# Optimization experiments

Hardware: AMD Instinct MI355X
Metric: run time of the kernel (lower is better)

## Reference

```python
import jax, jax.numpy as jnp
import numpy as np

N = 1500                 # number of proposals
NUM_CLASSES = 81         # COCO: background + 80
NMS_THRESH = 0.5
SCORE_THRESH = 0.05
MAX_DET = 100            # config.test.max_det
BBOX_REG_WEIGHTS = jnp.array([10.0, 10.0, 5.0, 5.0], dtype=jnp.float32)


def setup_inputs() -> dict:
    key = jax.random.key(0)
    k1, k2, k3 = jax.random.split(key, 3)
    H, W = 800.0, 1333.0
    # realistic proposals: random centers / sizes inside the image
    cx = jax.random.uniform(jax.random.fold_in(k1, 0), (N,)) * W
    cy = jax.random.uniform(jax.random.fold_in(k1, 1), (N,)) * H
    bw = jax.random.uniform(jax.random.fold_in(k1, 2), (N,)) * 200.0 + 16.0
    bh = jax.random.uniform(jax.random.fold_in(k1, 3), (N,)) * 200.0 + 16.0
    bottom_rois = jnp.stack(
        [jnp.zeros((N,)), cx - 0.5 * bw, cy - 0.5 * bh, cx + 0.5 * bw, cy + 0.5 * bh],
        axis=1).astype(jnp.float32)
    bbox_delta = (jax.random.normal(k2, (N, 4 * NUM_CLASSES)) * 0.5).astype(jnp.float32)
    cls_prob = jax.nn.softmax(jax.random.normal(k3, (N, NUM_CLASSES)) * 2.0, axis=-1).astype(jnp.float32)
    im_info = jnp.array([[H, W, 1.0]], dtype=jnp.float32)
    return {"bottom_rois": bottom_rois, "bbox_delta": bbox_delta,
            "cls_prob": cls_prob, "im_info": im_info}


def _decode_boxes(rois, deltas, im_info):
    # rois [N,4], deltas [N,4C] -> clipped boxes [N,C,4] (legacy +1 convention)
    x1, y1, x2, y2 = rois[:, 0], rois[:, 1], rois[:, 2], rois[:, 3]
    w = x2 - x1 + 1.0
    h = y2 - y1 + 1.0
    cx = x1 + 0.5 * w
    cy = y1 + 0.5 * h
    d = deltas.reshape(deltas.shape[0], -1, 4) / BBOX_REG_WEIGHTS  # [N,C,4]
    pcx = cx[:, None] + w[:, None] * d[..., 0]
    pcy = cy[:, None] + h[:, None] * d[..., 1]
    pw = w[:, None] * jnp.exp(d[..., 2])
    ph = h[:, None] * jnp.exp(d[..., 3])
    boxes = jnp.stack([pcx - 0.5 * pw, pcy - 0.5 * ph,
                       pcx + 0.5 * pw - 1.0, pcy + 0.5 * ph - 1.0], axis=-1)
    hw = im_info[0, :2]  # [height, width]
    lim = jnp.stack([hw[1] - 1.0, hw[0] - 1.0, hw[1] - 1.0, hw[0] - 1.0])
    return jnp.clip(boxes, 0.0, lim)


def _pairwise_iou(b):
    # b [N,4], legacy +1 areas (matches gpu_nms)
    x1, y1, x2, y2 = b[:, 0], b[:, 1], b[:, 2], b[:, 3]
    area = (x2 - x1 + 1.0) * (y2 - y1 + 1.0)
    iw = jnp.maximum(jnp.minimum(x2[:, None], x2[None, :]) - jnp.maximum(x1[:, None], x1[None, :]) + 1.0, 0.0)
    ih = jnp.maximum(jnp.minimum(y2[:, None], y2[None, :]) - jnp.maximum(y1[:, None], y1[None, :]) + 1.0, 0.0)
    inter = iw * ih
    return inter / (area[:, None] + area[None, :] - inter)


def _nms_one_class(boxes, scores):
    # boxes [N,4], scores [N] -> score-sorted boxes/scores + keep mask
    valid = scores > SCORE_THRESH
    order = jnp.argsort(-scores)
    b = boxes[order]
    s = scores[order]
    v = valid[order]
    iou = jax.lax.stop_gradient(_pairwise_iou(b))  # used only in comparisons

    def body(suppressed, i):
        keep_i = v[i] & ~suppressed[i]
        suppressed = suppressed | (keep_i & (iou[i] > NMS_THRESH))
        return suppressed, keep_i

    _, keep = jax.lax.scan(body, jnp.zeros((b.shape[0],), bool), jnp.arange(b.shape[0]))
    return b, s, keep


def reference(bottom_rois, bbox_delta, cls_prob, im_info):
    boxes = _decode_boxes(bottom_rois[:, 1:], bbox_delta, im_info)  # [N,C,4]
    C = cls_prob.shape[1]
    boxes_fg = jnp.swapaxes(boxes, 0, 1)[1:]   # [C-1,N,4]
    scores_fg = cls_prob.T[1:]                 # [C-1,N]
    b, s, keep = jax.vmap(_nms_one_class)(boxes_fg, scores_fg)
    # image-level max_det cap (>= kth score, as in source)
    flat = jnp.where(keep, s, -jnp.inf).reshape(-1)
    n_keep = keep.sum()
    kth = jax.lax.top_k(flat, MAX_DET)[0][-1]
    keep = keep & jnp.where(n_keep > MAX_DET, s >= kth, True)
    cls_idx = jnp.broadcast_to(jnp.arange(1, C)[:, None], s.shape)
    zeros = jnp.zeros_like(s[..., None])
    dets = jnp.concatenate([zeros, b, s[..., None]], axis=-1)  # [C-1,N,6]
    dets = jnp.where(keep[..., None], dets, 0.0).reshape(-1, 6)
    return dets, cls_idx.reshape(-1), keep.reshape(-1)
```

## Files before the change

kernel.cpp:

```cpp
#include <hip/hip_runtime.h>
#include <math.h>

#pragma clang fp contract(off)

#define N_ROIS     1500
#define NUM_CLS    81
#define FG         80
#define MAXC       1536
#define NMS_T      0.5f
#define SCORE_T    0.05f
#define MAX_DET    100
#define TOTAL      (FG * N_ROIS)
#define TPB        256
#define K1_BLOCKS  256
#define K2_TPB     1024
#define NCHUNK     ((N_ROIS + TPB - 1) / TPB)
#define SUBCAP     8192

__device__ __forceinline__ unsigned f2s(float f) {
    unsigned u = __float_as_uint(f);
    return (u & 0x80000000u) ? ~u : (u | 0x80000000u);
}
__device__ __forceinline__ float s2f(unsigned u) {
    return __uint_as_float((u & 0x80000000u) ? (u & 0x7FFFFFFFu) : ~u);
}

__global__ __launch_bounds__(TPB) void nms_k1(
    const float* __restrict__ rois,
    const float* __restrict__ deltas,
    const float* __restrict__ prob,
    const float* __restrict__ iminfo,
    float4* __restrict__ keptBox,
    int*    __restrict__ keptRow,
    float*  __restrict__ keptScore,
    int*    __restrict__ ctrs,
    float*  __restrict__ out)
{
    const int tid  = threadIdx.x;
    const int lane = tid & 63;
    const int wv   = tid >> 6;
    const int b    = blockIdx.x;

    if (b >= FG) {
        const float4 z4 = make_float4(0.f, 0.f, 0.f, 0.f);
        const int stride = (K1_BLOCKS - FG) * TPB;
        int g = (b - FG) * TPB + tid;

        float4* dets4 = (float4*)out;
        for (int i = g; i < TOTAL * 6 / 4; i += stride) dets4[i] = z4;

        float4* cls4  = (float4*)(out + (size_t)TOTAL * 6);
        float4* keep4 = (float4*)(out + (size_t)TOTAL * 7);
        for (int i = g; i < TOTAL / 4; i += stride) {
            float fc = (float)((i * 4) / N_ROIS + 1);
            cls4[i]  = make_float4(fc, fc, fc, fc);
            keep4[i] = z4;
        }
        return;
    }

    __shared__ unsigned long long key[MAXC];
    __shared__ unsigned long long skey[MAXC];
    __shared__ float4 box4[MAXC];
    __shared__ float  areaA[MAXC];
    __shared__ unsigned char keepf[MAXC], supp[MAXC];
    __shared__ int mcnt;

    const int c = b + 1;
    const int cbase = b * N_ROIS;

    if (tid == 0) mcnt = 0;
    __syncthreads();

    float sv[NCHUNK];
    #pragma unroll
    for (int t = 0; t < NCHUNK; ++t) {
        int i = t * TPB + tid;
        sv[t] = (i < N_ROIS) ? prob[i * NUM_CLS + c] : 0.0f;
    }
    #pragma unroll
    for (int t = 0; t < NCHUNK; ++t) {
        int i = t * TPB + tid;
        bool val = (i < N_ROIS) && (sv[t] > SCORE_T);
        unsigned long long m = __ballot(val);
        int base = 0;
        if (lane == 0 && m) base = atomicAdd(&mcnt, __popcll(m));
        base = __shfl(base, 0, 64);
        if (val) {
            int pos = base + __popcll(m & ((1ull << lane) - 1ull));
            key[pos] = ((unsigned long long)(~f2s(sv[t])) << 32) | (unsigned)i;
        }
    }
    __syncthreads();
    const int M = mcnt;
    if (M == 0) return;

    for (int i = tid; i < M; i += TPB) {
        unsigned long long kk = key[i];
        int cnt = 0;
        #pragma unroll 4
        for (int j = 0; j < M; ++j) cnt += (int)(key[j] < kk);
        skey[cnt] = kk;
    }
    __syncthreads();

    const float Hm1 = iminfo[0] - 1.0f;
    const float Wm1 = iminfo[1] - 1.0f;
    for (int k = tid; k < M; k += TPB) {
        unsigned long long kk = skey[k];
        int i = (int)(kk & 0xFFFFFFFFu);
        const float* rp = rois + i * 5;
        float x1 = rp[1], y1 = rp[2], x2 = rp[3], y2 = rp[4];
        float w  = x2 - x1 + 1.0f;
        float h  = y2 - y1 + 1.0f;
        float cx = x1 + 0.5f * w;
        float cy = y1 + 0.5f * h;
        const float* dp = deltas + i * (4 * NUM_CLS) + c * 4;
        float dx = dp[0] / 10.0f, dy = dp[1] / 10.0f;
        float dw = dp[2] / 5.0f,  dh = dp[3] / 5.0f;
        float pcx = cx + w * dx;
        float pcy = cy + h * dy;
        float pw  = w * expf(dw);
        float ph  = h * expf(dh);
        float a1 = pcx - 0.5f * pw;
        float a2 = pcy - 0.5f * ph;
        float a3 = pcx + 0.5f * pw - 1.0f;
        float a4 = pcy + 0.5f * ph - 1.0f;
        a1 = fminf(fmaxf(a1, 0.0f), Wm1);
        a2 = fminf(fmaxf(a2, 0.0f), Hm1);
        a3 = fminf(fmaxf(a3, 0.0f), Wm1);
        a4 = fminf(fmaxf(a4, 0.0f), Hm1);
        box4[k]  = make_float4(a1, a2, a3, a4);
        areaA[k] = (a3 - a1 + 1.0f) * (a4 - a2 + 1.0f);
        keepf[k] = 0; supp[k] = 0;
    }
    __syncthreads();

    const int MW = (M + 63) >> 6;
    const bool fast = (M * MW <= MAXC);

    if (fast) {
        for (int r = wv; r < M; r += TPB / 64) {
            float4 br = box4[r];
            float  ar = areaA[r];
            const int w0 = r >> 6;
            if (lane == 0)
                for (int w = 0; w < w0; ++w) key[r * MW + w] = 0ull;
            for (int w = w0; w < MW; ++w) {
                int col = (w << 6) | lane;
                bool inb = (col < M);
                int j = inb ? col : 0;
                float4 bj = box4[j];
                float  aj = areaA[j];
                float iw = fminf(br.z, bj.z) - fmaxf(br.x, bj.x) + 1.0f;
                float ih = fminf(br.w, bj.w) - fmaxf(br.y, bj.y) + 1.0f;
                iw = fmaxf(iw, 0.0f);
                ih = fmaxf(ih, 0.0f);
                float inter = iw * ih;
                float iou = inter / ((ar + aj) - inter);
                bool pred = inb && (col > r) && (iou > NMS_T);
                unsigned long long mk = __ballot(pred);
                if (lane == 0) key[r * MW + w] = mk;
            }
        }
        __syncthreads();

        if (tid < 64) {
            const int lw = (tid < MW) ? tid : 0;
            unsigned long long acc = 0;
            unsigned long long mcur = key[lw];
            for (int k = 0; k < M; ++k) {
                unsigned long long mnext =
                    (k + 1 < M) ? key[(k + 1) * MW + lw] : 0ull;
                int bit = (int)((acc >> (k & 63)) & 1ull);
                int sup = __shfl(bit, k >> 6, 64);
                if (!sup) {
                    acc |= mcur;
                    if (tid == 0) keepf[k] = 1;
                }
                mcur = mnext;
            }
        }
        __syncthreads();
    } else {
        for (int k = 0; k < M; ++k) {
            if (!supp[k]) {
                if (tid == 0) keepf[k] = 1;
                float4 bk = box4[k];
                float  ak = areaA[k];
                for (int j = k + 1 + tid; j < M; j += TPB) {
                    float4 bj = box4[j];
                    float  aj = areaA[j];
                    float iw = fminf(bk.z, bj.z) - fmaxf(bk.x, bj.x) + 1.0f;
                    float ih = fminf(bk.w, bj.w) - fmaxf(bk.y, bj.y) + 1.0f;
                    iw = fmaxf(iw, 0.0f);
                    ih = fmaxf(ih, 0.0f);
                    float inter = iw * ih;
                    float iou = inter / ((ak + aj) - inter);
                    if (iou > NMS_T) supp[j] = 1;
                }
            }
            __syncthreads();
        }
    }

    for (int k = tid; k < M; k += TPB) {
        if (keepf[k]) {
            int p = atomicAdd(&ctrs[0], 1);
            keptRow[p]   = cbase + k;
            keptBox[p]   = box4[k];
            keptScore[p] = s2f(~(unsigned)(skey[k] >> 32));
        }
    }
}

__global__ __launch_bounds__(K2_TPB) void kth_patch_k2(
    const int*    __restrict__ ctrs,
    const int*    __restrict__ keptRow,
    const float4* __restrict__ keptBox,
    const float*  __restrict__ keptScore,
    float* __restrict__ out)
{
    __shared__ int hist4[4][256];
    __shared__ unsigned sub[SUBCAP];
    __shared__ int wtot[4];
    __shared__ unsigned s_d0, s_sp;
    __shared__ int s_kk, s_cnt;
    __shared__ float s_kth;

    const int tid  = threadIdx.x;
    const int lane = tid & 63;
    const int wv   = tid >> 6;
    const int hp   = wv & 3;
    const int n = ctrs[0];

    if (n > MAX_DET) {
        if (tid < 1024) {
            #pragma unroll
            for (int w = 0; w < 4; ++w) if (tid < 256) hist4[w][tid] = 0;
        }
        __syncthreads();
        for (int i = tid; i < n; i += K2_TPB)
            atomicAdd(&hist4[hp][f2s(keptScore[i]) >> 24], 1);
        __syncthreads();
        if (tid < 256) {
            const int h = hist4[0][tid] + hist4[1][tid] +
                          hist4[2][tid] + hist4[3][tid];
            int r = h;
            #pragma unroll
            for (int off = 1; off < 64; off <<= 1) {
                int o = __shfl_down(r, off, 64);
                if (lane + off < 64) r += o;
            }
            if (lane == 0) wtot[wv] = r;
        }
        __syncthreads();
        if (tid < 256) {
            const int h = hist4[0][tid] + hist4[1][tid] +
                          hist4[2][tid] + hist4[3][tid];
            int r = h;
            #pragma unroll
            for (int off = 1; off < 64; off <<= 1) {
                int o = __shfl_down(r, off, 64);
                if (lane + off < 64) r += o;
            }
            int hi = 0;
            #pragma unroll
            for (int w2 = 0; w2 < 4; ++w2) if (w2 > wv) hi += wtot[w2];
            const int S_ge = r + hi, S_gt = S_ge - h;
            if (S_gt < MAX_DET && S_ge >= MAX_DET) {
                s_d0 = (unsigned)tid;
                s_kk = MAX_DET - S_gt;
            }
        }
        if (tid == 0) { s_cnt = 0; s_sp = 0u; }
        __syncthreads();
        const unsigned d0 = s_d0;

        for (int i0 = 0; i0 < n; i0 += K2_TPB) {
            int i = i0 + tid;
            unsigned u = (i < n) ? f2s(keptScore[i]) : 0u;
            bool match = (i < n) && ((u >> 24) == d0);
            unsigned long long m = __ballot(match);
            int base = 0;
            if (lane == 0 && m) base = atomicAdd(&s_cnt, __popcll(m));
            base = __shfl(base, 0, 64);
            if (match) {
                int pos = base + __popcll(m & ((1ull << lane) - 1ull));
                if (pos < SUBCAP) sub[pos] = u & 0xFFFFFFu;
            }
        }
        __syncthreads();
        const int ns = s_cnt;
        const bool inLds = (ns <= SUBCAP);
        const int limit = inLds ? ns : n;

        for (int d = 1; d < 4; ++d) {
            const int shift = 24 - 8 * d;
            if (tid < 256) {
                #pragma unroll
                for (int w = 0; w < 4; ++w) hist4[w][tid] = 0;
            }
            __syncthreads();
            const unsigned sp = s_sp;
            for (int i = tid; i < limit; i += K2_TPB) {
                unsigned v; bool ok;
                if (inLds) { v = sub[i]; ok = true; }
                else {
                    unsigned u = f2s(keptScore[i]);
                    ok = ((u >> 24) == d0);
                    v = u & 0xFFFFFFu;
                }
                if (ok && (d == 1 || (v >> (shift + 8)) == sp))
                    atomicAdd(&hist4[hp][(v >> shift) & 255u], 1);
            }
            __syncthreads();
            if (tid < 256) {
                const int h = hist4[0][tid] + hist4[1][tid] +
                              hist4[2][tid] + hist4[3][tid];
                int r = h;
                #pragma unroll
                for (int off = 1; off < 64; off <<= 1) {
                    int o = __shfl_down(r, off, 64);
                    if (lane + off < 64) r += o;
                }
                if (lane == 0) wtot[wv] = r;
            }
            __syncthreads();
            if (tid < 256) {
                const int h = hist4[0][tid] + hist4[1][tid] +
                              hist4[2][tid] + hist4[3][tid];
                int r = h;
                #pragma unroll
                for (int off = 1; off < 64; off <<= 1) {
                    int o = __shfl_down(r, off, 64);
                    if (lane + off < 64) r += o;
                }
                int hi = 0;
                #pragma unroll
                for (int w2 = 0; w2 < 4; ++w2) if (w2 > wv) hi += wtot[w2];
                const int S_ge = r + hi, S_gt = S_ge - h;
                const int kk = s_kk;
                if (S_gt < kk && S_ge >= kk) {
                    s_sp = (s_sp << 8) | (unsigned)tid;
                    s_kk = kk - S_gt;
                }
            }
            __syncthreads();
        }
        if (tid == 0) s_kth = s2f((s_d0 << 24) | s_sp);
    } else {
        if (tid == 0) s_kth = -INFINITY;
    }
    __syncthreads();
    const float kth = s_kth;

    for (int i = tid; i < n; i += K2_TPB) {
        float s = keptScore[i];
        if (s >= kth) {
            int r = keptRow[i];
            float4 b4 = keptBox[i];
            float* dst = out + (size_t)r * 6;
            dst[1] = b4.x; dst[2] = b4.y; dst[3] = b4.z; dst[4] = b4.w; dst[5] = s;
            out[(size_t)TOTAL * 7 + r] = 1.0f;
        }
    }
}

extern "C" void kernel_launch(void* const* d_in, const int* in_sizes, int n_in,
                              void* d_out, int out_size, void* d_ws, size_t ws_size,
                              hipStream_t stream) {
    const float* rois   = (const float*)d_in[0];
    const float* deltas = (const float*)d_in[1];
    const float* prob   = (const float*)d_in[2];
    const float* iminfo = (const float*)d_in[3];
    float* out = (float*)d_out;

    float4* keptBox   = (float4*)d_ws;
    int*    keptRow   = (int*)(keptBox + TOTAL);
    float*  keptScore = (float*)(keptRow + TOTAL);
    int*    ctrs      = (int*)(keptScore + TOTAL);

    hipMemsetAsync(ctrs, 0, sizeof(int), stream);
    nms_k1<<<K1_BLOCKS, TPB, 0, stream>>>(rois, deltas, prob, iminfo,
                                          keptBox, keptRow, keptScore, ctrs, out);
    kth_patch_k2<<<1, K2_TPB, 0, stream>>>(ctrs, keptRow, keptBox, keptScore, out);
}
```

Before: 104.4 us.

## Use per-class kept segments and drop global atomic counter and memset

Each class block now writes its kept detections into its own fixed segment and records a per-class count, replacing the global atomic counter and the host memset launch. The kth-score kernel builds prefix offsets from these counts, stages all score bits in LDS when they fit, and runs a uniform 4-pass radix select over them. This removes one memset launch and global atomic contention. In exchange, the single-block second kernel now walks 80 segments serially, and the final scatter loops per class, so threads sit idle when segments are small.

```diff
diff --git a/kernel.cpp b/kernel.cpp
--- a/kernel.cpp
+++ b/kernel.cpp
@@ -15,7 +15,8 @@
 #define K1_BLOCKS  256
 #define K2_TPB     1024
 #define NCHUNK     ((N_ROIS + TPB - 1) / TPB)
-#define SUBCAP     8192
+#define SEGW       1500
+#define DENSECAP   8192
 
 __device__ __forceinline__ unsigned f2s(float f) {
     unsigned u = __float_as_uint(f);
@@ -33,7 +34,7 @@
     float4* __restrict__ keptBox,
     int*    __restrict__ keptRow,
     float*  __restrict__ keptScore,
-    int*    __restrict__ ctrs,
+    int*    __restrict__ kcnt,
     float*  __restrict__ out)
 {
     const int tid  = threadIdx.x;
@@ -64,12 +65,12 @@
     __shared__ float4 box4[MAXC];
     __shared__ float  areaA[MAXC];
     __shared__ unsigned char keepf[MAXC], supp[MAXC];
-    __shared__ int mcnt;
+    __shared__ int mcnt, kloc;
 
     const int c = b + 1;
     const int cbase = b * N_ROIS;
 
-    if (tid == 0) mcnt = 0;
+    if (tid == 0) { mcnt = 0; kloc = 0; }
     __syncthreads();
 
     float sv[NCHUNK];
@@ -93,7 +94,10 @@
     }
     __syncthreads();
     const int M = mcnt;
-    if (M == 0) return;
+    if (M == 0) {
+        if (tid == 0) kcnt[b] = 0;
+        return;
+    }
 
     for (int i = tid; i < M; i += TPB) {
         unsigned long long kk = key[i];
@@ -204,115 +208,86 @@
         }
     }
 
+    const int segb = b * SEGW;
     for (int k = tid; k < M; k += TPB) {
         if (keepf[k]) {
-            int p = atomicAdd(&ctrs[0], 1);
-            keptRow[p]   = cbase + k;
-            keptBox[p]   = box4[k];
-            keptScore[p] = s2f(~(unsigned)(skey[k] >> 32));
-        }
-    }
+            int p = atomicAdd(&kloc, 1);
+            keptRow[segb + p]   = cbase + k;
+            keptBox[segb + p]   = box4[k];
+            keptScore[segb + p] = s2f(~(unsigned)(skey[k] >> 32));
+        }
+    }
+    __syncthreads();
+    if (tid == 0) kcnt[b] = kloc;
 }
 
 __global__ __launch_bounds__(K2_TPB) void kth_patch_k2(
-    const int*    __restrict__ ctrs,
+    const int*    __restrict__ kcnt,
     const int*    __restrict__ keptRow,
     const float4* __restrict__ keptBox,
     const float*  __restrict__ keptScore,
     float* __restrict__ out)
 {
+    __shared__ int cnts[FG];
+    __shared__ int offs[FG + 1];
     __shared__ int hist4[4][256];
-    __shared__ unsigned sub[SUBCAP];
+    __shared__ unsigned sbits[DENSECAP];
     __shared__ int wtot[4];
-    __shared__ unsigned s_d0, s_sp;
-    __shared__ int s_kk, s_cnt;
+    __shared__ unsigned s_pref;
+    __shared__ int s_kk;
     __shared__ float s_kth;
 
     const int tid  = threadIdx.x;
     const int lane = tid & 63;
     const int wv   = tid >> 6;
     const int hp   = wv & 3;
-    const int n = ctrs[0];
+
+    if (tid < FG) cnts[tid] = kcnt[tid];
+    __syncthreads();
+    if (tid == 0) {
+        int acc = 0;
+        #pragma unroll 8
+        for (int b2 = 0; b2 < FG; ++b2) { offs[b2] = acc; acc += cnts[b2]; }
+        offs[FG] = acc;
+    }
+    __syncthreads();
+    const int n = offs[FG];
 
     if (n > MAX_DET) {
-        if (tid < 1024) {
-            #pragma unroll
-            for (int w = 0; w < 4; ++w) if (tid < 256) hist4[w][tid] = 0;
-        }
+        const bool dense = (n <= DENSECAP);
+        if (dense) {
+            for (int b2 = 0; b2 < FG; ++b2) {
+                const int cb = cnts[b2], ob = offs[b2], gb = b2 * SEGW;
+                for (int i = tid; i < cb; i += K2_TPB)
+                    sbits[ob + i] = f2s(keptScore[gb + i]);
+            }
+        }
+        if (tid == 0) { s_pref = 0u; s_kk = MAX_DET; }
         __syncthreads();
-        for (int i = tid; i < n; i += K2_TPB)
-            atomicAdd(&hist4[hp][f2s(keptScore[i]) >> 24], 1);
-        __syncthreads();
-        if (tid < 256) {
-            const int h = hist4[0][tid] + hist4[1][tid] +
-                          hist4[2][tid] + hist4[3][tid];
-            int r = h;
-            #pragma unroll
-            for (int off = 1; off < 64; off <<= 1) {
-                int o = __shfl_down(r, off, 64);
-                if (lane + off < 64) r += o;
-            }
-            if (lane == 0) wtot[wv] = r;
-        }
-        __syncthreads();
-        if (tid < 256) {
-            const int h = hist4[0][tid] + hist4[1][tid] +
-                          hist4[2][tid] + hist4[3][tid];
-            int r = h;
-            #pragma unroll
-            for (int off = 1; off < 64; off <<= 1) {
-                int o = __shfl_down(r, off, 64);
-                if (lane + off < 64) r += o;
-            }
-            int hi = 0;
-            #pragma unroll
-            for (int w2 = 0; w2 < 4; ++w2) if (w2 > wv) hi += wtot[w2];
-            const int S_ge = r + hi, S_gt = S_ge - h;
-            if (S_gt < MAX_DET && S_ge >= MAX_DET) {
-                s_d0 = (unsigned)tid;
-                s_kk = MAX_DET - S_gt;
-            }
-        }
-        if (tid == 0) { s_cnt = 0; s_sp = 0u; }
-        __syncthreads();
-        const unsigned d0 = s_d0;
-
-        for (int i0 = 0; i0 < n; i0 += K2_TPB) {
-            int i = i0 + tid;
-            unsigned u = (i < n) ? f2s(keptScore[i]) : 0u;
-            bool match = (i < n) && ((u >> 24) == d0);
-            unsigned long long m = __ballot(match);
-            int base = 0;
-            if (lane == 0 && m) base = atomicAdd(&s_cnt, __popcll(m));
-            base = __shfl(base, 0, 64);
-            if (match) {
-                int pos = base + __popcll(m & ((1ull << lane) - 1ull));
-                if (pos < SUBCAP) sub[pos] = u & 0xFFFFFFu;
-            }
-        }
-        __syncthreads();
-        const int ns = s_cnt;
-        const bool inLds = (ns <= SUBCAP);
-        const int limit = inLds ? ns : n;
-
-        for (int d = 1; d < 4; ++d) {
+
+        for (int d = 0; d < 4; ++d) {
             const int shift = 24 - 8 * d;
             if (tid < 256) {
                 #pragma unroll
                 for (int w = 0; w < 4; ++w) hist4[w][tid] = 0;
             }
             __syncthreads();
-            const unsigned sp = s_sp;
-            for (int i = tid; i < limit; i += K2_TPB) {
-                unsigned v; bool ok;
-                if (inLds) { v = sub[i]; ok = true; }
-                else {
-                    unsigned u = f2s(keptScore[i]);
-                    ok = ((u >> 24) == d0);
-                    v = u & 0xFFFFFFu;
-                }
-                if (ok && (d == 1 || (v >> (shift + 8)) == sp))
-                    atomicAdd(&hist4[hp][(v >> shift) & 255u], 1);
+            const unsigned pref = s_pref;
+            if (dense) {
+                for (int i = tid; i < n; i += K2_TPB) {
+                    unsigned u = sbits[i];
+                    if (d == 0 || (u >> (shift + 8)) == pref)
+                        atomicAdd(&hist4[hp][(u >> shift) & 255u], 1);
+                }
+            } else {
+                for (int b2 = 0; b2 < FG; ++b2) {
+                    const int cb = cnts[b2], gb = b2 * SEGW;
+                    for (int i = tid; i < cb; i += K2_TPB) {
+                        unsigned u = f2s(keptScore[gb + i]);
+                        if (d == 0 || (u >> (shift + 8)) == pref)
+                            atomicAdd(&hist4[hp][(u >> shift) & 255u], 1);
+                    }
+                }
             }
             __syncthreads();
             if (tid < 256) {
@@ -342,27 +317,31 @@
                 const int S_ge = r + hi, S_gt = S_ge - h;
                 const int kk = s_kk;
                 if (S_gt < kk && S_ge >= kk) {
-                    s_sp = (s_sp << 8) | (unsigned)tid;
-                    s_kk = kk - S_gt;
-                }
-            }
-            __syncthreads();
-        }
-        if (tid == 0) s_kth = s2f((s_d0 << 24) | s_sp);
+                    s_pref = (pref << 8) | (unsigned)tid;
+                    s_kk   = kk - S_gt;
+                }
+            }
+            __syncthreads();
+        }
+        if (tid == 0) s_kth = s2f(s_pref);
     } else {
         if (tid == 0) s_kth = -INFINITY;
     }
     __syncthreads();
     const float kth = s_kth;
 
-    for (int i = tid; i < n; i += K2_TPB) {
-        float s = keptScore[i];
-        if (s >= kth) {
-            int r = keptRow[i];
-            float4 b4 = keptBox[i];
-            float* dst = out + (size_t)r * 6;
-            dst[1] = b4.x; dst[2] = b4.y; dst[3] = b4.z; dst[4] = b4.w; dst[5] = s;
-            out[(size_t)TOTAL * 7 + r] = 1.0f;
+    for (int b2 = 0; b2 < FG; ++b2) {
+        const int cb = cnts[b2], gb = b2 * SEGW;
+        for (int i = tid; i < cb; i += K2_TPB) {
+            float s = keptScore[gb + i];
+            if (s >= kth) {
+                int r = keptRow[gb + i];
+                float4 b4 = keptBox[gb + i];
+                float* dst = out + (size_t)r * 6;
+                dst[1] = b4.x; dst[2] = b4.y; dst[3] = b4.z;
+                dst[4] = b4.w; dst[5] = s;
+                out[(size_t)TOTAL * 7 + r] = 1.0f;
+            }
         }
     }
 }
@@ -377,12 +356,11 @@
     float* out = (float*)d_out;
 
     float4* keptBox   = (float4*)d_ws;
-    int*    keptRow   = (int*)(keptBox + TOTAL);
-    float*  keptScore = (float*)(keptRow + TOTAL);
-    int*    ctrs      = (int*)(keptScore + TOTAL);
-
-    hipMemsetAsync(ctrs, 0, sizeof(int), stream);
+    int*    keptRow   = (int*)(keptBox + FG * SEGW);
+    float*  keptScore = (float*)(keptRow + FG * SEGW);
+    int*    kcnt      = (int*)(keptScore + FG * SEGW);
+
     nms_k1<<<K1_BLOCKS, TPB, 0, stream>>>(rois, deltas, prob, iminfo,
-                                          keptBox, keptRow, keptScore, ctrs, out);
-    kth_patch_k2<<<1, K2_TPB, 0, stream>>>(ctrs, keptRow, keptBox, keptScore, out);
-}
+                                          keptBox, keptRow, keptScore, kcnt, out);
+    kth_patch_k2<<<1, K2_TPB, 0, stream>>>(kcnt, keptRow, keptBox, keptScore, out);
+}
```

Result: slower. 161.9 us (+55.1%).
